# Optimization experiments

Hardware: AMD Instinct MI355X
Metric: run time of the kernel (lower is better)

Reference implementation:

```python
import jax, jax.numpy as jnp
import numpy as np

KS = 2        # kernel_size
DIL = 1       # dilation
FILTERS = 512
Z_DIM = 128
B, C, T = 8, 512, 4096
TZ = T + 2 * (KS - 1)


def _conv1d(x, w, b):
    # x: (B, L, Cin), w: (ks, Cin, Cout) -> VALID conv, channels-last (keras Conv1D)
    y = jax.lax.conv_general_dilated(x, w, window_strides=(1,), padding='VALID',
                                     dimension_numbers=('NWC', 'WIO', 'NWC'))
    return y + b


def _adaptor(z, w1, b1, w2, b2):
    return _conv1d(jax.nn.relu(_conv1d(z, w1, b1)), w2, b2)


def setup_inputs() -> dict:
    key = jax.random.key(0)
    ks = jax.random.split(key, 10)
    lim = np.sqrt(6.0 / FILTERS)
    u = lambda k, shp: jax.random.uniform(k, shp, jnp.float32, -lim, lim)
    return {
        'x': jax.random.normal(ks[0], (B, C, T), jnp.float32),
        'z': jax.random.normal(ks[1], (B, TZ, Z_DIM), jnp.float32),
        'ww1': u(ks[2], (KS, Z_DIM, FILTERS)), 'wb1': jnp.zeros((FILTERS,), jnp.float32),
        'ww2': u(ks[3], (KS, FILTERS, FILTERS)), 'wb2': jnp.zeros((FILTERS,), jnp.float32),
        'bw1': u(ks[4], (KS, Z_DIM, FILTERS)), 'bb1': jnp.zeros((FILTERS,), jnp.float32),
        'bw2': u(ks[5], (KS, FILTERS, FILTERS)), 'bb2': jnp.zeros((FILTERS,), jnp.float32),
    }


def reference(x, z, ww1, wb1, ww2, wb2, bw1, bb1, bw2, bb2):
    m = x.shape[1]
    t = x.shape[2]
    pad = DIL * (KS - 1)
    xp = jnp.pad(x, ((0, 0), (0, 0), (0, pad)))
    end = t + pad
    # im2col-style unfold: (B, C*KS, T)
    xu = jnp.concatenate([xp[:, :, pad - i * DIL: end - i * DIL] for i in range(KS)], axis=1)
    weights = _adaptor(z, ww1, wb1, ww2, wb2)   # (B, T, F)
    bias = _adaptor(z, bw1, bb1, bw2, bb2)      # (B, T, F)
    y = jnp.matmul(xu, weights)                 # (B, C*KS, F)
    return y[:, :m, :] + bias[:, :m, :]
```

## Files before the change

kernel.cpp:

```cpp
#include <hip/hip_runtime.h>

typedef short short8 __attribute__((ext_vector_type(8)));
typedef float float4v __attribute__((ext_vector_type(4)));
typedef __attribute__((address_space(1))) const unsigned int gu32;
typedef __attribute__((address_space(3))) unsigned int lu32;

__device__ __forceinline__ unsigned short f2bf(float f) {
  unsigned int u = __builtin_bit_cast(unsigned int, f);
  u += 0x7FFFu + ((u >> 16) & 1u);
  return (unsigned short)(u >> 16);
}
__device__ __forceinline__ float bf2f(unsigned short s) {
  return __builtin_bit_cast(float, (unsigned int)s << 16);
}

__global__ __launch_bounds__(256) void prep_w(
    const float* __restrict__ ww1, const float* __restrict__ ww2,
    const float* __restrict__ bw1, const float* __restrict__ bw2,
    const float* __restrict__ z,
    unsigned short* __restrict__ w1T, unsigned short* __restrict__ w2T,
    unsigned short* __restrict__ b1T, unsigned short* __restrict__ b2T,
    unsigned short* __restrict__ zb)
{
  int i = blockIdx.x * 256 + threadIdx.x;
  if (i < 131072) {
    int n = i & 511, k = i >> 9;
    w1T[n * 256 + k] = f2bf(ww1[i]);
  } else if (i < 655360) {
    int j = i - 131072; int n = j & 511, k = j >> 9;
    w2T[n * 1024 + k] = f2bf(ww2[j]);
  } else if (i < 786432) {
    int j = i - 655360; int n = j & 511, k = j >> 9;
    b1T[n * 256 + k] = f2bf(bw1[j]);
  } else if (i < 1310720) {
    int j = i - 786432; int n = j & 511, k = j >> 9;
    b2T[n * 1024 + k] = f2bf(bw2[j]);
  } else {
    int j = i - 1310720;
    zb[j] = f2bf(z[j]);
  }
}

template<int BM, int BN, bool RELU, bool OBF16, bool TRANS, bool SPLITK, int NH, bool ROWPACK>
__device__ __forceinline__ void gemm_core(
    int bx, int by, int bz, int nzTot, unsigned short* smem,
    const unsigned short* __restrict__ A,
    const unsigned short* __restrict__ A2,
    const unsigned short* __restrict__ Bt,
    const float* __restrict__ biasv,
    void* __restrict__ outp,
    void* __restrict__ outp2,
    int M, int Kchunk, int RPB, int EXTRA, int BSCALE,
    int nHalf, int bRowMask,
    long long bStrideB, long long outBatchStride, int outLd)
{
  constexpr int WM = BM / 2, WN = BN / 2;
  constexpr int NI = WM / 16, NJ = WN / 16;
  constexpr int AI = BM / 64;
  constexpr int BI = BN / 64;
  constexpr int SA1 = BM * 32, SB1 = BN * 32;
  unsigned short* sB0 = smem + NH * SA1;

  const int tid  = threadIdx.x;
  const int lane = tid & 63;
  const int wave = tid >> 6;
  const int wm = wave >> 1, wn = wave & 1;
  const int lr = lane & 15, quad = lane >> 4;

  const int r0 = bx * BM;
  const int n0 = by * BN;
  const int bb = r0 / RPB;
  const int Ktot = SPLITK ? Kchunk * nzTot : Kchunk;
  const int kOff = SPLITK ? bz * Kchunk : 0;
  const long long bOffB = (long long)bb * bStrideB;
  const unsigned short* Ae = (nHalf && n0 >= nHalf) ? A2 : A;

  const int srow = lane >> 2;
  const int sg = (lane & 3) ^ (srow & 3);
  const unsigned short* gA[AI]; unsigned short* ldsA[AI];
#pragma unroll
  for (int c = 0; c < AI; ++c) {
    int instr = c * 4 + wave;
    int row = instr * 16 + srow;
    int r = r0 + row; if (r > M - 1) r = M - 1;
    gA[c] = Ae + ((long long)r + (long long)(r / RPB) * EXTRA) * BSCALE + kOff + sg * 8;
    ldsA[c] = smem + instr * 512;
  }
  const unsigned short* gB[BI]; unsigned short* ldsB[BI];
#pragma unroll
  for (int c = 0; c < BI; ++c) {
    int instr = c * 4 + wave;
    int row = instr * 16 + srow;
    gB[c] = Bt + (long long)((n0 + row) & bRowMask) * Ktot + bOffB + kOff + sg * 8;
    ldsB[c] = sB0 + instr * 512;
  }

  int aoff[NI], boff[NJ];
#pragma unroll
  for (int i = 0; i < NI; ++i) {
    int rr = wm * WM + i * 16 + lr;
    aoff[i] = rr * 32 + ((quad ^ (rr & 3)) * 8);
  }
#pragma unroll
  for (int j = 0; j < NJ; ++j) {
    int rr = wn * WN + j * 16 + lr;
    boff[j] = rr * 32 + ((quad ^ (rr & 3)) * 8);
  }

  float4v acc[NI][NJ];
  const float4v z4 = {0.f, 0.f, 0.f, 0.f};
#pragma unroll
  for (int i = 0; i < NI; ++i)
#pragma unroll
    for (int j = 0; j < NJ; ++j) acc[i][j] = z4;

  for (int k0 = 0; k0 < Kchunk; k0 += 32 * NH) {
#pragma unroll
    for (int h = 0; h < NH; ++h) {
#pragma unroll
      for (int c = 0; c < AI; ++c)
        __builtin_amdgcn_global_load_lds((gu32*)(gA[c] + k0 + h * 32),
                                         (lu32*)(ldsA[c] + h * SA1), 16, 0, 0);
#pragma unroll
      for (int c = 0; c < BI; ++c)
        __builtin_amdgcn_global_load_lds((gu32*)(gB[c] + k0 + h * 32),
                                         (lu32*)(ldsB[c] + h * SB1), 16, 0, 0);
    }
    __syncthreads();
#pragma unroll
    for (int h = 0; h < NH; ++h) {
      short8 af[NI], bfr[NJ];
#pragma unroll
      for (int i = 0; i < NI; ++i) af[i] = *(const short8*)(smem + h * SA1 + aoff[i]);
#pragma unroll
      for (int j = 0; j < NJ; ++j) bfr[j] = *(const short8*)(sB0 + h * SB1 + boff[j]);
#pragma unroll
      for (int i = 0; i < NI; ++i)
#pragma unroll
        for (int j = 0; j < NJ; ++j)
          acc[i][j] = __builtin_amdgcn_mfma_f32_16x16x32_bf16(af[i], bfr[j], acc[i][j], 0, 0, 0);
    }
    __syncthreads();
  }

  if (TRANS) {
    unsigned short* Ts = smem;
#pragma unroll
    for (int j = 0; j < NJ; ++j) {
      int fr = wn * WN + j * 16 + lr;
      float bv = biasv[n0 + fr];
#pragma unroll
      for (int i = 0; i < NI; ++i) {
        int tr = wm * WM + i * 16 + quad * 4;
        unsigned long long pk = 0;
#pragma unroll
        for (int g = 0; g < 4; ++g) {
          float vv = acc[i][j][g] + bv;
          if (RELU) vv = fmaxf(vv, 0.f);
          pk |= (unsigned long long)f2bf(vv) << (16 * g);
        }
        *(unsigned long long*)(Ts + fr * 136 + tr) = pk;
      }
    }
    __syncthreads();
    int fr = tid >> 1, sgg = tid & 1;
    int t0l = r0 - bb * RPB;
    unsigned short* dst = (unsigned short*)outp + (long long)bb * outBatchStride
                        + (long long)(n0 + fr) * outLd + t0l + sgg * 64;
    const unsigned short* srcp = Ts + fr * 136 + sgg * 64;
#pragma unroll
    for (int u = 0; u < 8; ++u)
      *(uint4*)(dst + u * 8) = *(const uint4*)(srcp + u * 8);
  } else if (ROWPACK) {
    void* op = (SPLITK && bz) ? outp2 : outp;
    unsigned short* R = smem;
#pragma unroll
    for (int j = 0; j < NJ; ++j) {
      int cc = wn * WN + j * 16 + lr;
#pragma unroll
      for (int i = 0; i < NI; ++i) {
        int rrb = wm * WM + i * 16 + quad * 4;
#pragma unroll
        for (int g = 0; g < 4; ++g)
          R[(rrb + g) * 136 + cc] = f2bf(acc[i][j][g]);
      }
    }
    __syncthreads();
    int rloc = tid >> 1, half = tid & 1;
    unsigned short* dstp = (unsigned short*)op + (long long)(r0 + rloc) * outLd + n0 + half * 64;
    const unsigned short* srcp = R + rloc * 136 + half * 64;
#pragma unroll
    for (int u = 0; u < 8; ++u)
      *(uint4*)(dstp + u * 8) = *(const uint4*)(srcp + u * 8);
  } else {
    void* op = (SPLITK && bz) ? outp2 : outp;
#pragma unroll
    for (int j = 0; j < NJ; ++j) {
      int n_g = n0 + wn * WN + j * 16 + lr;
      float bv = biasv ? biasv[n_g] : 0.f;
#pragma unroll
      for (int i = 0; i < NI; ++i) {
        int r_base = r0 + wm * WM + i * 16 + quad * 4;
#pragma unroll
        for (int g = 0; g < 4; ++g) {
          int r_g = r_base + g;
          if (r_g >= M) continue;
          float v = acc[i][j][g] + bv;
          if (RELU) v = fmaxf(v, 0.f);
          long long oidx = (long long)r_g * outLd + n_g;
          if (OBF16) ((unsigned short*)op)[oidx] = f2bf(v);
          else       ((float*)op)[oidx] = v;
        }
      }
    }
  }
}

template<int BM, int BN, bool RELU, bool OBF16, bool TRANS, bool SPLITK, int NH, bool ROWPACK>
__global__ __launch_bounds__(256)
void gemm_bt(const unsigned short* __restrict__ A,
             const unsigned short* __restrict__ A2,
             const unsigned short* __restrict__ Bt,
             const float* __restrict__ biasv,
             void* __restrict__ outp,
             void* __restrict__ outp2,
             int M, int Kchunk, int RPB, int EXTRA, int BSCALE,
             int nHalf, int bRowMask,
             long long bStrideB, long long outBatchStride, int outLd)
{
  constexpr int STAGE = NH * (BM * 32 + BN * 32);
  constexpr int REPK = (TRANS || ROWPACK) ? 128 * 136 : 0;
  constexpr int SMEMN = (REPK > STAGE) ? REPK : STAGE;
  __shared__ unsigned short smem[SMEMN];
  gemm_core<BM, BN, RELU, OBF16, TRANS, SPLITK, NH, ROWPACK>(
      blockIdx.x, blockIdx.y, blockIdx.z, gridDim.z, smem,
      A, A2, Bt, biasv, outp, outp2,
      M, Kchunk, RPB, EXTRA, BSCALE, nHalf, bRowMask,
      bStrideB, outBatchStride, outLd);
}

__global__ __launch_bounds__(256) void mega(
    const float* __restrict__ x,
    const unsigned short* __restrict__ zb,
    const unsigned short* __restrict__ w1T,
    const unsigned short* __restrict__ b1T,
    const float* __restrict__ wb1,
    const float* __restrict__ bb1,
    unsigned short* __restrict__ h1T,
    unsigned short* __restrict__ h1b,
    unsigned short* __restrict__ xs,
    unsigned short* __restrict__ xz,
    float* __restrict__ rs)
{
  __shared__ unsigned short smem[17408];
  int b = blockIdx.x;
  if (b < 1024) {
    gemm_core<128, 128, true, true, true, false, 2, false>(
        b & 255, b >> 8, 0, 1, smem,
        zb, nullptr, w1T, wb1, h1T, nullptr,
        32768, 256, 4096, 2, 128, 0, 0xFFFF, 0, 512ll * 4096, 4096);
  } else if (b < 1284) {
    int idx = b - 1024;
    gemm_core<64, 128, true, true, false, false, 2, false>(
        idx % 65, idx / 65, 0, 1, smem,
        zb, nullptr, b1T, bb1, h1b, nullptr,
        4104, 256, 513, 3585, 128, 0, 0xFFFF, 0, 0, 512);
  } else {
    float* red = (float*)smem;
    long long r = b - 1284;
    const float* xr = x + r * 4096;
    int t0 = threadIdx.x * 16;
    float v[17];
    const float4* xr4 = (const float4*)(xr + t0);
#pragma unroll
    for (int q = 0; q < 4; ++q) {
      float4 f = xr4[q];
      v[q * 4] = f.x; v[q * 4 + 1] = f.y; v[q * 4 + 2] = f.z; v[q * 4 + 3] = f.w;
    }
    v[16] = (t0 + 16 < 4096) ? xr[t0 + 16] : 0.f;
    unsigned int spk[8], zpk[8];
    float sum = 0.f;
#pragma unroll
    for (int q = 0; q < 8; ++q) {
      unsigned short s0 = f2bf(v[2 * q + 1]);
      unsigned short s1 = f2bf(v[2 * q + 2]);
      sum += bf2f(s0);
      sum += bf2f(s1);
      spk[q] = (unsigned int)s0 | ((unsigned int)s1 << 16);
      unsigned short z0 = (t0 == 0 && q == 0) ? (unsigned short)0 : f2bf(v[2 * q]);
      unsigned short z1 = f2bf(v[2 * q + 1]);
      zpk[q] = (unsigned int)z0 | ((unsigned int)z1 << 16);
    }
    *(uint4*)(xs + r * 4096 + t0)     = *(uint4*)(spk);
    *(uint4*)(xs + r * 4096 + t0 + 8) = *(uint4*)(spk + 4);
    *(uint4*)(xz + r * 4096 + t0)     = *(uint4*)(zpk);
    *(uint4*)(xz + r * 4096 + t0 + 8) = *(uint4*)(zpk + 4);
#pragma unroll
    for (int off = 32; off > 0; off >>= 1) sum += __shfl_down(sum, off);
    if ((threadIdx.x & 63) == 0) red[threadIdx.x >> 6] = sum;
    __syncthreads();
    if (threadIdx.x == 0) rs[r] = red[0] + red[1] + red[2] + red[3];
  }
}

__global__ __launch_bounds__(256) void final_gemm3(
    const unsigned short* __restrict__ p0,
    const unsigned short* __restrict__ p1,
    const unsigned short* __restrict__ h1b,
    const unsigned short* __restrict__ w2T,
    const unsigned short* __restrict__ b2T,
    const float* __restrict__ rs,
    const float* __restrict__ wb2,
    const float* __restrict__ bb2,
    float* __restrict__ out)
{
  constexpr int SA1 = 64 * 32, SB1 = 64 * 32;
  __shared__ unsigned short smem[4 * SA1 + 4 * SB1];
  const int tid = threadIdx.x;
  const int lane = tid & 63, wave = tid >> 6;
  const int wm = wave >> 1, wn = wave & 1;
  const int lr = lane & 15, quad = lane >> 4;
  const int r0 = blockIdx.x * 64, n0 = blockIdx.y * 64;

  const int srow = lane >> 2;
  const int sg = (lane & 3) ^ (srow & 3);
  const int row = wave * 16 + srow;
  const int rA = r0 + row;
  const int rB = n0 + row;
  const unsigned short* aP[3] = {
    p0 + (long long)rA * 1024 + sg * 8,
    p1 + (long long)rA * 1024 + sg * 8,
    h1b + ((long long)rA + (rA >> 9)) * 512 + sg * 8 };
  const unsigned short* bP[3] = {
    w2T + (long long)rB * 1024 + sg * 8,
    w2T + (long long)rB * 1024 + sg * 8,
    b2T + (long long)rB * 1024 + sg * 8 };
  unsigned short* ldsA = smem + wave * 512;
  unsigned short* ldsB = smem + 4 * SA1 + wave * 512;

  int aoff[2], boff[2];
#pragma unroll
  for (int i = 0; i < 2; ++i) {
    int rr = wm * 32 + i * 16 + lr;
    aoff[i] = rr * 32 + ((quad ^ (rr & 3)) * 8);
    int nn = wn * 32 + i * 16 + lr;
    boff[i] = 4 * SA1 + nn * 32 + ((quad ^ (nn & 3)) * 8);
  }

  float4v acc[2][2];
  const float4v z4 = {0.f, 0.f, 0.f, 0.f};
  acc[0][0] = z4; acc[0][1] = z4; acc[1][0] = z4; acc[1][1] = z4;

  for (int k0 = 0; k0 < 3072; k0 += 128) {
    int seg = k0 >> 10;
    int kk = k0 & 1023;
#pragma unroll
    for (int h = 0; h < 4; ++h) {
      __builtin_amdgcn_global_load_lds((gu32*)(aP[seg] + kk + h * 32),
                                       (lu32*)(ldsA + h * SA1), 16, 0, 0);
      __builtin_amdgcn_global_load_lds((gu32*)(bP[seg] + kk + h * 32),
                                       (lu32*)(ldsB + h * SB1), 16, 0, 0);
    }
    __syncthreads();
#pragma unroll
    for (int h = 0; h < 4; ++h) {
      short8 af[2], bfr[2];
      af[0] = *(const short8*)(smem + h * SA1 + aoff[0]);
      af[1] = *(const short8*)(smem + h * SA1 + aoff[1]);
      bfr[0] = *(const short8*)(smem + h * SB1 + boff[0]);
      bfr[1] = *(const short8*)(smem + h * SB1 + boff[1]);
#pragma unroll
      for (int i = 0; i < 2; ++i)
#pragma unroll
        for (int j = 0; j < 2; ++j)
          acc[i][j] = __builtin_amdgcn_mfma_f32_16x16x32_bf16(af[i], bfr[j], acc[i][j], 0, 0, 0);
    }
    __syncthreads();
  }

#pragma unroll
  for (int j = 0; j < 2; ++j) {
    int n_g = n0 + wn * 32 + j * 16 + lr;
    float w2b = wb2[n_g], bbv = bb2[n_g];
#pragma unroll
    for (int i = 0; i < 2; ++i) {
      int rb = r0 + wm * 32 + i * 16 + quad * 4;
#pragma unroll
      for (int g = 0; g < 4; ++g) {
        int r_g = rb + g;
        out[(long long)r_g * 512 + n_g] = acc[i][j][g] + rs[r_g] * w2b + bbv;
      }
    }
  }
}

extern "C" void kernel_launch(void* const* d_in, const int* in_sizes, int n_in,
                              void* d_out, int out_size, void* d_ws, size_t ws_size,
                              hipStream_t stream) {
  const float* x   = (const float*)d_in[0];
  const float* z   = (const float*)d_in[1];
  const float* ww1 = (const float*)d_in[2];
  const float* wb1 = (const float*)d_in[3];
  const float* ww2 = (const float*)d_in[4];
  const float* wb2 = (const float*)d_in[5];
  const float* bw1 = (const float*)d_in[6];
  const float* bb1 = (const float*)d_in[7];
  const float* bw2 = (const float*)d_in[8];
  const float* bb2 = (const float*)d_in[9];

  char* ws = (char*)d_ws;
  unsigned short* xs  = (unsigned short*)ws; ws += 16777216ll * 2;
  unsigned short* xz  = (unsigned short*)ws; ws += 16777216ll * 2;
  unsigned short* zb  = (unsigned short*)ws; ws += 4196352ll  * 2;
  unsigned short* h1T = (unsigned short*)ws; ws += 16777216ll * 2;
  unsigned short* h1b = (unsigned short*)ws; ws += 2101248ll  * 2;
  unsigned short* w2T = (unsigned short*)ws; ws += 524288ll * 2;
  unsigned short* b2T = (unsigned short*)ws; ws += 524288ll * 2;
  float* rs = (float*)ws;                    ws += 4096ll * 4;
  char* tail = ws;
  unsigned short* w1T = (unsigned short*)tail;
  unsigned short* b1T = (unsigned short*)tail + 131072;
  unsigned short* p0  = zb;
  unsigned short* p1  = (unsigned short*)tail;

  prep_w<<<21512, 256, 0, stream>>>(ww1, ww2, bw1, bw2, z, w1T, w2T, b1T, b2T, zb);
  mega<<<5380, 256, 0, stream>>>(x, zb, w1T, b1T, wb1, bb1, h1T, h1b, xs, xz, rs);
  gemm_bt<128, 128, false, true, false, true, 4, true><<<dim3(32, 8, 2), 256, 0, stream>>>(
      xs, xz, h1T, nullptr, p0, p1,
      4096, 2048, 512, 0, 4096, 512, 511, 512ll * 4096, 0, 1024);
  final_gemm3<<<dim3(64, 8), 256, 0, stream>>>(
      p0, p1, h1b, w2T, b2T, rs, wb2, bb2, (float*)d_out);
}
```

Measured before the change: 254.4 us.

## Shrink LDS footprint: halve transpose staging, single k-stage in mega, narrower split-K tiles

The transposed epilogue now writes one half of the N columns at a time into a half-size LDS buffer, with an extra barrier per pass. This lets the mega kernel's shared array shrink from 17408 to 8704 shorts, and its GEMM branches drop from two k-sub-stages per iteration to one. The split-K GEMM switches from 128x128 tiles with NH=4 to 128x64 tiles with NH=2 and twice as many blocks. The ROWPACK epilogue is generalised to the new BN. The aim is higher occupancy and more parallel blocks, at the cost of more barriers and less K work per synchronisation.

```diff
diff --git a/kernel.cpp b/kernel.cpp
--- a/kernel.cpp
+++ b/kernel.cpp
@@ -145,33 +145,42 @@
 
   if (TRANS) {
     unsigned short* Ts = smem;
-#pragma unroll
-    for (int j = 0; j < NJ; ++j) {
-      int fr = wn * WN + j * 16 + lr;
-      float bv = biasv[n0 + fr];
-#pragma unroll
-      for (int i = 0; i < NI; ++i) {
-        int tr = wm * WM + i * 16 + quad * 4;
-        unsigned long long pk = 0;
-#pragma unroll
-        for (int g = 0; g < 4; ++g) {
-          float vv = acc[i][j][g] + bv;
-          if (RELU) vv = fmaxf(vv, 0.f);
-          pk |= (unsigned long long)f2bf(vv) << (16 * g);
+    const int t0l = r0 - bb * RPB;
+#pragma unroll
+    for (int p = 0; p < 2; ++p) {
+      if (wn == p) {
+#pragma unroll
+        for (int j = 0; j < NJ; ++j) {
+          int frl = j * 16 + lr;
+          float bv = biasv[n0 + p * WN + frl];
+#pragma unroll
+          for (int i = 0; i < NI; ++i) {
+            int tr = wm * WM + i * 16 + quad * 4;
+            unsigned long long pk = 0;
+#pragma unroll
+            for (int g = 0; g < 4; ++g) {
+              float vv = acc[i][j][g] + bv;
+              if (RELU) vv = fmaxf(vv, 0.f);
+              pk |= (unsigned long long)f2bf(vv) << (16 * g);
+            }
+            *(unsigned long long*)(Ts + frl * (BM + 8) + tr) = pk;
+          }
         }
-        *(unsigned long long*)(Ts + fr * 136 + tr) = pk;
       }
-    }
-    __syncthreads();
-    int fr = tid >> 1, sgg = tid & 1;
-    int t0l = r0 - bb * RPB;
-    unsigned short* dst = (unsigned short*)outp + (long long)bb * outBatchStride
-                        + (long long)(n0 + fr) * outLd + t0l + sgg * 64;
-    const unsigned short* srcp = Ts + fr * 136 + sgg * 64;
-#pragma unroll
-    for (int u = 0; u < 8; ++u)
-      *(uint4*)(dst + u * 8) = *(const uint4*)(srcp + u * 8);
+      __syncthreads();
+      int frl = tid >> 2, sgg = tid & 3;
+      unsigned short* dst = (unsigned short*)outp + (long long)bb * outBatchStride
+                          + (long long)(n0 + p * WN + frl) * outLd + t0l + sgg * (BM / 4);
+      const unsigned short* srcp = Ts + frl * (BM + 8) + sgg * (BM / 4);
+#pragma unroll
+      for (int u = 0; u < BM / 32; ++u)
+        *(uint4*)(dst + u * 8) = *(const uint4*)(srcp + u * 8);
+      __syncthreads();
+    }
   } else if (ROWPACK) {
+    constexpr int BNP = BN + 8;
+    constexpr int TPR = 256 / BM;
+    constexpr int EPT = BN / TPR;
     void* op = (SPLITK && bz) ? outp2 : outp;
     unsigned short* R = smem;
 #pragma unroll
@@ -182,15 +191,15 @@
         int rrb = wm * WM + i * 16 + quad * 4;
 #pragma unroll
         for (int g = 0; g < 4; ++g)
-          R[(rrb + g) * 136 + cc] = f2bf(acc[i][j][g]);
+          R[(rrb + g) * BNP + cc] = f2bf(acc[i][j][g]);
       }
     }
     __syncthreads();
-    int rloc = tid >> 1, half = tid & 1;
-    unsigned short* dstp = (unsigned short*)op + (long long)(r0 + rloc) * outLd + n0 + half * 64;
-    const unsigned short* srcp = R + rloc * 136 + half * 64;
-#pragma unroll
-    for (int u = 0; u < 8; ++u)
+    int rloc = tid / TPR, part = tid % TPR;
+    unsigned short* dstp = (unsigned short*)op + (long long)(r0 + rloc) * outLd + n0 + part * EPT;
+    const unsigned short* srcp = R + rloc * BNP + part * EPT;
+#pragma unroll
+    for (int u = 0; u < EPT / 8; ++u)
       *(uint4*)(dstp + u * 8) = *(const uint4*)(srcp + u * 8);
   } else {
     void* op = (SPLITK && bz) ? outp2 : outp;
@@ -229,7 +238,7 @@
              long long bStrideB, long long outBatchStride, int outLd)
 {
   constexpr int STAGE = NH * (BM * 32 + BN * 32);
-  constexpr int REPK = (TRANS || ROWPACK) ? 128 * 136 : 0;
+  constexpr int REPK = TRANS ? (BN / 2) * (BM + 8) : (ROWPACK ? BM * (BN + 8) : 0);
   constexpr int SMEMN = (REPK > STAGE) ? REPK : STAGE;
   __shared__ unsigned short smem[SMEMN];
   gemm_core<BM, BN, RELU, OBF16, TRANS, SPLITK, NH, ROWPACK>(
@@ -252,16 +261,16 @@
     unsigned short* __restrict__ xz,
     float* __restrict__ rs)
 {
-  __shared__ unsigned short smem[17408];
+  __shared__ unsigned short smem[8704];
   int b = blockIdx.x;
   if (b < 1024) {
-    gemm_core<128, 128, true, true, true, false, 2, false>(
+    gemm_core<128, 128, true, true, true, false, 1, false>(
         b & 255, b >> 8, 0, 1, smem,
         zb, nullptr, w1T, wb1, h1T, nullptr,
         32768, 256, 4096, 2, 128, 0, 0xFFFF, 0, 512ll * 4096, 4096);
   } else if (b < 1284) {
     int idx = b - 1024;
-    gemm_core<64, 128, true, true, false, false, 2, false>(
+    gemm_core<64, 128, true, true, false, false, 1, false>(
         idx % 65, idx / 65, 0, 1, smem,
         zb, nullptr, b1T, bb1, h1b, nullptr,
         4104, 256, 513, 3585, 128, 0, 0xFFFF, 0, 0, 512);
@@ -425,7 +434,7 @@
 
   prep_w<<<21512, 256, 0, stream>>>(ww1, ww2, bw1, bw2, z, w1T, w2T, b1T, b2T, zb);
   mega<<<5380, 256, 0, stream>>>(x, zb, w1T, b1T, wb1, bb1, h1T, h1b, xs, xz, rs);
-  gemm_bt<128, 128, false, true, false, true, 4, true><<<dim3(32, 8, 2), 256, 0, stream>>>(
+  gemm_bt<128, 64, false, true, false, true, 2, true><<<dim3(32, 16, 2), 256, 0, stream>>>(
       xs, xz, h1T, nullptr, p0, p1,
       4096, 2048, 512, 0, 4096, 512, 511, 512ll * 4096, 0, 1024);
   final_gemm3<<<dim3(64, 8), 256, 0, stream>>>(
```

New measurement: 259.9 us. 2.2% more time.
